# Optimization experiments

Measured on AMD Instinct MI355X. Metric: run time of the kernel, lower is better.

The kernel has to match this reference:

```python
import jax, jax.numpy as jnp
import numpy as np

HASHMAP_SIZES = [65536, 262144]
HASHMAP_DIM = 4
RESO = 2097152
OUTPUT_DIM = 48


def setup_inputs() -> dict:
    key = jax.random.key(0)
    k1, k2, k3, k4 = jax.random.split(key, 4)
    total = sum(HASHMAP_SIZES)
    # codes initialized uniform(-1, 1) as in torch.nn.init.uniform_
    codes = jax.random.uniform(k1, (total, HASHMAP_DIM), dtype=jnp.float32, minval=-1.0, maxval=1.0)
    # bias-free linear head: stored as [in, out] so forward is feats @ W
    fan_in = len(HASHMAP_SIZES) * HASHMAP_DIM
    W = jax.random.normal(k2, (fan_in, OUTPUT_DIM), dtype=jnp.float32) / np.sqrt(fan_in)
    map_65536 = jax.random.randint(k3, (RESO, HASHMAP_DIM), 0, 65536, dtype=jnp.int64) if jax.config.jax_enable_x64 else jax.random.randint(k3, (RESO, HASHMAP_DIM), 0, 65536, dtype=jnp.int32)
    map_262144 = jax.random.randint(k4, (RESO, HASHMAP_DIM), 0, 262144, dtype=jnp.int32)
    return {"codes": codes, "W": W, "map_65536": map_65536, "map_262144": map_262144}


def _gather_level(code, idx_map):
    # code: [size, dim]; idx_map: [reso, dim]; out[n, i] = code[idx_map[n, i], i]
    dim_idx = jnp.arange(code.shape[1])[None, :]  # [1, dim]
    return code[idx_map, dim_idx]  # [reso, dim]


def reference(codes, W, map_65536, map_262144):
    # split stacked codebook into per-level tables
    code0 = codes[: HASHMAP_SIZES[0]]                      # [65536, 4]
    code1 = codes[HASHMAP_SIZES[0] : HASHMAP_SIZES[0] + HASHMAP_SIZES[1]]  # [262144, 4]
    out0 = _gather_level(code0, map_65536)    # [RESO, 4]
    out1 = _gather_level(code1, map_262144)   # [RESO, 4]
    feats = jnp.concatenate([out0, out1], axis=1)  # [RESO, 8]
    return feats @ W  # [RESO, 48]
```

## Files before the change

kernel.cpp:

```cpp
#include <hip/hip_runtime.h>


#define RESO    2097152
#define OUT_DIM 48
#define LVL0    65536
#define NCODES  327680
#define BLK     192
#define TILE    256
#define NITER   16
#define TPB     4
#define NBLK    (RESO / (TILE * TPB))

typedef int            vi4 __attribute__((ext_vector_type(4)));
typedef float          vf4 __attribute__((ext_vector_type(4)));
typedef unsigned short vu4 __attribute__((ext_vector_type(4)));

static __device__ __forceinline__ unsigned short f2bf_rne(float x) {
    unsigned int u = __float_as_uint(x);
    u += 0x7fffu + ((u >> 16) & 1u);
    return (unsigned short)(u >> 16);
}
static __device__ __forceinline__ float bf2f(unsigned short h) {
    return __uint_as_float(((unsigned int)h) << 16);
}

static __device__ __forceinline__ void barrier_lds_only() {
    __builtin_amdgcn_sched_barrier(0);
    asm volatile("s_waitcnt lgkmcnt(0)" ::: "memory");
    __builtin_amdgcn_s_barrier();
    __builtin_amdgcn_sched_barrier(0);
}

__global__ __launch_bounds__(256) void convert_kernel(
    const float* __restrict__ codes, unsigned short* __restrict__ bf)
{
    const int i = blockIdx.x * 256 + threadIdx.x;
    const vf4 v = ((const vf4*)codes)[i];
    vu4 o;
    o.x = f2bf_rne(v.x); o.y = f2bf_rne(v.y);
    o.z = f2bf_rne(v.z); o.w = f2bf_rne(v.w);
    ((vu4*)bf)[i] = o;
}

__global__ __launch_bounds__(BLK) void gshash_pipe_kernel(
    const unsigned short* __restrict__ tab,
    const float* __restrict__ W,
    const vi4*   __restrict__ map0,
    const vi4*   __restrict__ map1,
    float*       __restrict__ out)
{
    __shared__ float feats[2][TILE * 8];

    const int t     = threadIdx.x;
    const int col4  = t % 12;
    const int rbase = t / 12;

    vf4 Wv[8];
    #pragma unroll
    for (int k = 0; k < 8; ++k)
        Wv[k] = ((const vf4*)(W + k * OUT_DIM))[col4];

    const unsigned short* __restrict__ t1 = tab + LVL0 * 4;
    const size_t row00 = (size_t)blockIdx.x * (TPB * TILE);

    vi4 m0b[2], m1b[2], n0b[2], n1b[2];
    unsigned short g[16];

    #define LOADMAPS(j, s) {                                                  \
        const size_t r0 = row00 + (size_t)(j) * TILE;                         \
        m0b[s] = __builtin_nontemporal_load(&map0[r0 + t]);                   \
        m1b[s] = __builtin_nontemporal_load(&map1[r0 + t]);                   \
        if (t < TILE - BLK) {                                                 \
            n0b[s] = __builtin_nontemporal_load(&map0[r0 + BLK + t]);         \
            n1b[s] = __builtin_nontemporal_load(&map1[r0 + BLK + t]);         \
        } }

    #define GATHERS(s) {                                                      \
        g[0] = tab[m0b[s].x * 4 + 0];                                         \
        g[1] = tab[m0b[s].y * 4 + 1];                                         \
        g[2] = tab[m0b[s].z * 4 + 2];                                         \
        g[3] = tab[m0b[s].w * 4 + 3];                                         \
        g[4] = t1[m1b[s].x * 4 + 0];                                          \
        g[5] = t1[m1b[s].y * 4 + 1];                                          \
        g[6] = t1[m1b[s].z * 4 + 2];                                          \
        g[7] = t1[m1b[s].w * 4 + 3];                                          \
        if (t < TILE - BLK) {                                                 \
            g[8]  = tab[n0b[s].x * 4 + 0];                                    \
            g[9]  = tab[n0b[s].y * 4 + 1];                                    \
            g[10] = tab[n0b[s].z * 4 + 2];                                    \
            g[11] = tab[n0b[s].w * 4 + 3];                                    \
            g[12] = t1[n1b[s].x * 4 + 0];                                     \
            g[13] = t1[n1b[s].y * 4 + 1];                                     \
            g[14] = t1[n1b[s].z * 4 + 2];                                     \
            g[15] = t1[n1b[s].w * 4 + 3];                                     \
        } }

    #define LDSWRITE(buf) {                                                   \
        vf4 a, b;                                                             \
        a.x = bf2f(g[0]); a.y = bf2f(g[1]); a.z = bf2f(g[2]); a.w = bf2f(g[3]); \
        b.x = bf2f(g[4]); b.y = bf2f(g[5]); b.z = bf2f(g[6]); b.w = bf2f(g[7]); \
        *(vf4*)&feats[buf][t * 8]     = a;                                    \
        *(vf4*)&feats[buf][t * 8 + 4] = b;                                    \
        if (t < TILE - BLK) {                                                 \
            vf4 c, d;                                                         \
            c.x = bf2f(g[8]);  c.y = bf2f(g[9]);  c.z = bf2f(g[10]); c.w = bf2f(g[11]); \
            d.x = bf2f(g[12]); d.y = bf2f(g[13]); d.z = bf2f(g[14]); d.w = bf2f(g[15]); \
            *(vf4*)&feats[buf][(BLK + t) * 8]     = c;                        \
            *(vf4*)&feats[buf][(BLK + t) * 8 + 4] = d;                        \
        } }

    LOADMAPS(0, 0);
    LOADMAPS(1, 1);
    GATHERS(0);
    LDSWRITE(0);
    barrier_lds_only();

    #pragma unroll
    for (int i = 0; i < TPB; ++i) {
        const int cur = i & 1;

        if (i + 2 < TPB) LOADMAPS(i + 2, cur);
        if (i + 1 < TPB) GATHERS(cur ^ 1);

        vf4* __restrict__ out4 = (vf4*)(out + (row00 + (size_t)i * TILE) * OUT_DIM);
        #pragma unroll
        for (int j = 0; j < NITER; ++j) {
            const int r = j * 16 + rbase;
            const vf4 fa = *(const vf4*)&feats[cur][r * 8];
            const vf4 fb = *(const vf4*)&feats[cur][r * 8 + 4];
            vf4 acc = fa.x * Wv[0];
            acc += fa.y * Wv[1];
            acc += fa.z * Wv[2];
            acc += fa.w * Wv[3];
            acc += fb.x * Wv[4];
            acc += fb.y * Wv[5];
            acc += fb.z * Wv[6];
            acc += fb.w * Wv[7];
            __builtin_nontemporal_store(acc, &out4[j * BLK + t]);
        }

        if (i + 1 < TPB) {
            LDSWRITE(cur ^ 1);
            barrier_lds_only();
        }
    }
    #undef LOADMAPS
    #undef GATHERS
    #undef LDSWRITE
}

__global__ __launch_bounds__(BLK) void gshash_f32_kernel(
    const float* __restrict__ codes,
    const float* __restrict__ W,
    const vi4*   __restrict__ map0,
    const vi4*   __restrict__ map1,
    float*       __restrict__ out)
{
    __shared__ float feats[TILE * 8];
    const int t     = threadIdx.x;
    const int col4  = t % 12;
    const int rbase = t / 12;
    const size_t row0 = (size_t)blockIdx.x * TILE;

    vf4 Wv[8];
    #pragma unroll
    for (int k = 0; k < 8; ++k)
        Wv[k] = ((const vf4*)(W + k * OUT_DIM))[col4];

    const float* __restrict__ c1 = codes + LVL0 * 4;
    #pragma unroll
    for (int half = 0; half < 2; ++half) {
        const int r = half * BLK + t;
        if (half == 0 || t < TILE - BLK) {
            const vi4 m0 = __builtin_nontemporal_load(&map0[row0 + r]);
            const vi4 m1 = __builtin_nontemporal_load(&map1[row0 + r]);
            vf4 a, b;
            a.x = codes[m0.x * 4 + 0];
            a.y = codes[m0.y * 4 + 1];
            a.z = codes[m0.z * 4 + 2];
            a.w = codes[m0.w * 4 + 3];
            b.x = c1[m1.x * 4 + 0];
            b.y = c1[m1.y * 4 + 1];
            b.z = c1[m1.z * 4 + 2];
            b.w = c1[m1.w * 4 + 3];
            *(vf4*)&feats[r * 8]     = a;
            *(vf4*)&feats[r * 8 + 4] = b;
        }
    }
    __syncthreads();

    vf4* __restrict__ out4 = (vf4*)(out + row0 * OUT_DIM);
    #pragma unroll
    for (int j = 0; j < NITER; ++j) {
        const int r = j * 16 + rbase;
        const vf4 fa = *(const vf4*)&feats[r * 8];
        const vf4 fb = *(const vf4*)&feats[r * 8 + 4];
        vf4 acc = fa.x * Wv[0];
        acc += fa.y * Wv[1];
        acc += fa.z * Wv[2];
        acc += fa.w * Wv[3];
        acc += fb.x * Wv[4];
        acc += fb.y * Wv[5];
        acc += fb.z * Wv[6];
        acc += fb.w * Wv[7];
        __builtin_nontemporal_store(acc, &out4[j * BLK + t]);
    }
}

extern "C" void kernel_launch(void* const* d_in, const int* in_sizes, int n_in,
                              void* d_out, int out_size, void* d_ws, size_t ws_size,
                              hipStream_t stream) {
    const float* codes = (const float*)d_in[0];
    const float* W     = (const float*)d_in[1];
    const vi4*   map0  = (const vi4*)d_in[2];
    const vi4*   map1  = (const vi4*)d_in[3];
    float*       out   = (float*)d_out;

    const size_t tab_bytes = (size_t)NCODES * 4 * sizeof(unsigned short);

    if (ws_size >= tab_bytes) {
        unsigned short* tab = (unsigned short*)d_ws;
        convert_kernel<<<NCODES / 256, 256, 0, stream>>>(codes, tab);
        gshash_pipe_kernel<<<NBLK, BLK, 0, stream>>>(tab, W, map0, map1, out);
    } else {
        gshash_f32_kernel<<<RESO / TILE, BLK, 0, stream>>>(codes, W, map0, map1, out);
    }
}
```

Measured before the change: 149.4 us.

## Deepen gather pipeline to two tiles ahead and double tiles per block

Doubles the number of 256-row tiles each block processes and deepens the software pipeline so map loads run three tiles ahead and codebook gathers two tiles ahead, using two register buffers for gathered values. The aim is to hide more random-gather latency behind the matmul and output stores. In exchange it halves the block count, which reduces grid-level parallelism, and raises register pressure, which may lower occupancy.

```diff
diff --git a/kernel.cpp b/kernel.cpp
--- a/kernel.cpp
+++ b/kernel.cpp
@@ -8,7 +8,7 @@
 #define BLK     192
 #define TILE    256
 #define NITER   16
-#define TPB     4
+#define TPB     8
 #define NBLK    (RESO / (TILE * TPB))
 
 typedef int            vi4 __attribute__((ext_vector_type(4)));
@@ -63,8 +63,8 @@
     const unsigned short* __restrict__ t1 = tab + LVL0 * 4;
     const size_t row00 = (size_t)blockIdx.x * (TPB * TILE);
 
-    vi4 m0b[2], m1b[2], n0b[2], n1b[2];
-    unsigned short g[16];
+    vi4 m0b[3], m1b[3], n0b[3], n1b[3];
+    unsigned short gA[16], gB[16];
 
     #define LOADMAPS(j, s) {                                                  \
         const size_t r0 = row00 + (size_t)(j) * TILE;                         \
@@ -75,52 +75,57 @@
             n1b[s] = __builtin_nontemporal_load(&map1[r0 + BLK + t]);         \
         } }
 
-    #define GATHERS(s) {                                                      \
-        g[0] = tab[m0b[s].x * 4 + 0];                                         \
-        g[1] = tab[m0b[s].y * 4 + 1];                                         \
-        g[2] = tab[m0b[s].z * 4 + 2];                                         \
-        g[3] = tab[m0b[s].w * 4 + 3];                                         \
-        g[4] = t1[m1b[s].x * 4 + 0];                                          \
-        g[5] = t1[m1b[s].y * 4 + 1];                                          \
-        g[6] = t1[m1b[s].z * 4 + 2];                                          \
-        g[7] = t1[m1b[s].w * 4 + 3];                                          \
+    #define GATHERS(s, G) {                                                   \
+        G[0] = tab[m0b[s].x * 4 + 0];                                         \
+        G[1] = tab[m0b[s].y * 4 + 1];                                         \
+        G[2] = tab[m0b[s].z * 4 + 2];                                         \
+        G[3] = tab[m0b[s].w * 4 + 3];                                         \
+        G[4] = t1[m1b[s].x * 4 + 0];                                          \
+        G[5] = t1[m1b[s].y * 4 + 1];                                          \
+        G[6] = t1[m1b[s].z * 4 + 2];                                          \
+        G[7] = t1[m1b[s].w * 4 + 3];                                          \
         if (t < TILE - BLK) {                                                 \
-            g[8]  = tab[n0b[s].x * 4 + 0];                                    \
-            g[9]  = tab[n0b[s].y * 4 + 1];                                    \
-            g[10] = tab[n0b[s].z * 4 + 2];                                    \
-            g[11] = tab[n0b[s].w * 4 + 3];                                    \
-            g[12] = t1[n1b[s].x * 4 + 0];                                     \
-            g[13] = t1[n1b[s].y * 4 + 1];                                     \
-            g[14] = t1[n1b[s].z * 4 + 2];                                     \
-            g[15] = t1[n1b[s].w * 4 + 3];                                     \
+            G[8]  = tab[n0b[s].x * 4 + 0];                                    \
+            G[9]  = tab[n0b[s].y * 4 + 1];                                    \
+            G[10] = tab[n0b[s].z * 4 + 2];                                    \
+            G[11] = tab[n0b[s].w * 4 + 3];                                    \
+            G[12] = t1[n1b[s].x * 4 + 0];                                     \
+            G[13] = t1[n1b[s].y * 4 + 1];                                     \
+            G[14] = t1[n1b[s].z * 4 + 2];                                     \
+            G[15] = t1[n1b[s].w * 4 + 3];                                     \
         } }
 
-    #define LDSWRITE(buf) {                                                   \
+    #define LDSWRITE(G, buf) {                                                \
         vf4 a, b;                                                             \
-        a.x = bf2f(g[0]); a.y = bf2f(g[1]); a.z = bf2f(g[2]); a.w = bf2f(g[3]); \
-        b.x = bf2f(g[4]); b.y = bf2f(g[5]); b.z = bf2f(g[6]); b.w = bf2f(g[7]); \
+        a.x = bf2f(G[0]); a.y = bf2f(G[1]); a.z = bf2f(G[2]); a.w = bf2f(G[3]); \
+        b.x = bf2f(G[4]); b.y = bf2f(G[5]); b.z = bf2f(G[6]); b.w = bf2f(G[7]); \
         *(vf4*)&feats[buf][t * 8]     = a;                                    \
         *(vf4*)&feats[buf][t * 8 + 4] = b;                                    \
         if (t < TILE - BLK) {                                                 \
             vf4 c, d;                                                         \
-            c.x = bf2f(g[8]);  c.y = bf2f(g[9]);  c.z = bf2f(g[10]); c.w = bf2f(g[11]); \
-            d.x = bf2f(g[12]); d.y = bf2f(g[13]); d.z = bf2f(g[14]); d.w = bf2f(g[15]); \
+            c.x = bf2f(G[8]);  c.y = bf2f(G[9]);  c.z = bf2f(G[10]); c.w = bf2f(G[11]); \
+            d.x = bf2f(G[12]); d.y = bf2f(G[13]); d.z = bf2f(G[14]); d.w = bf2f(G[15]); \
             *(vf4*)&feats[buf][(BLK + t) * 8]     = c;                        \
             *(vf4*)&feats[buf][(BLK + t) * 8 + 4] = d;                        \
         } }
 
     LOADMAPS(0, 0);
     LOADMAPS(1, 1);
-    GATHERS(0);
-    LDSWRITE(0);
+    LOADMAPS(2, 2);
+    GATHERS(0, gA);
+    LDSWRITE(gA, 0);
+    GATHERS(1, gB);
     barrier_lds_only();
 
     #pragma unroll
     for (int i = 0; i < TPB; ++i) {
         const int cur = i & 1;
 
-        if (i + 2 < TPB) LOADMAPS(i + 2, cur);
-        if (i + 1 < TPB) GATHERS(cur ^ 1);
+        if (i + 3 < TPB) LOADMAPS(i + 3, (i + 3) % 3);
+        if (i + 2 < TPB) {
+            if (((i + 2) & 1) == 0) { GATHERS((i + 2) % 3, gA); }
+            else                    { GATHERS((i + 2) % 3, gB); }
+        }
 
         vf4* __restrict__ out4 = (vf4*)(out + (row00 + (size_t)i * TILE) * OUT_DIM);
         #pragma unroll
@@ -140,7 +145,8 @@
         }
 
         if (i + 1 < TPB) {
-            LDSWRITE(cur ^ 1);
+            if (((i + 1) & 1) == 0) { LDSWRITE(gA, 0); }
+            else                    { LDSWRITE(gB, 1); }
             barrier_lds_only();
         }
     }
```

After: 140.8 us. 1.06x faster.
